# Kernel optimization log

Measured on AMD Instinct MI355X. Metric: run time of the kernel, lower is better.

## Reference

```python
import jax, jax.numpy as jnp
import numpy as np

L, B, D, H = 2048, 2, 1024, 16
DK = D // H
SCALE = DK ** -0.5


def setup_inputs() -> dict:
    key = jax.random.key(0)
    ks = jax.random.split(key, 11)
    w_std = D ** -0.5
    return {
        "query": jax.random.normal(ks[0], (L, B, D), dtype=jnp.float32),
        "key": jax.random.normal(ks[1], (L, B, D), dtype=jnp.float32),
        "value": jax.random.normal(ks[2], (L, B, D), dtype=jnp.float32),
        "WQ_w": jax.random.normal(ks[3], (D, D), dtype=jnp.float32) * w_std,
        "WQ_b": jnp.zeros((D,), dtype=jnp.float32),
        "WK_w": jax.random.normal(ks[4], (D, D), dtype=jnp.float32) * w_std,
        "WK_b": jnp.zeros((D,), dtype=jnp.float32),
        "WV_w": jax.random.normal(ks[5], (D, D), dtype=jnp.float32) * w_std,
        "WV_b": jnp.zeros((D,), dtype=jnp.float32),
        "WO_w": jax.random.normal(ks[6], (D, D), dtype=jnp.float32) * w_std,
        "WO_b": jnp.zeros((D,), dtype=jnp.float32),
    }


def reference(query, key, value, WQ_w, WQ_b, WK_w, WK_b, WV_w, WV_b, WO_w, WO_b):
    tgt_len, batch, _ = query.shape
    src_len = key.shape[0]
    # linear projections (torch Linear: x @ W^T + b)
    q = (query @ WQ_w.T + WQ_b) * SCALE            # [L, B, D]
    k = key @ WK_w.T + WK_b                        # [S, B, D]
    v = value @ WV_w.T + WV_b                      # [S, B, D]
    # split heads: [len, B, D] -> [B*H, len, DK]
    q = q.reshape(tgt_len, batch * H, DK).transpose(1, 0, 2)
    k = k.reshape(src_len, batch * H, DK).transpose(1, 0, 2)
    v = v.reshape(src_len, batch * H, DK).transpose(1, 0, 2)
    # attention scores and softmax (full [B*H, L, S] matrix, as in the original)
    scores = jnp.einsum('nld,nsd->nls', q, k)      # [B*H, L, S]
    probs = jax.nn.softmax(scores, axis=-1)
    out = jnp.einsum('nls,nsd->nld', probs, v)     # [B*H, L, DK]
    # merge heads: [B*H, L, DK] -> [L, B, D]
    out = out.transpose(1, 0, 2).reshape(tgt_len, batch, D)
    return out @ WO_w.T + WO_b
```

## Files before the change

kernel.cpp:

```cpp
#include <hip/hip_runtime.h>
#include <hip/hip_fp16.h>

#define LL 2048
#define BB 2
#define DD 1024
#define HH 16
#define DKK 64

typedef _Float16 h8 __attribute__((ext_vector_type(8)));
typedef _Float16 h4 __attribute__((ext_vector_type(4)));
typedef float f4 __attribute__((ext_vector_type(4)));
typedef float f16v __attribute__((ext_vector_type(16)));

#define BAR() do {                                              \
    asm volatile("s_waitcnt lgkmcnt(0)" ::: "memory");          \
    __builtin_amdgcn_s_barrier();                               \
    asm volatile("" ::: "memory");                              \
} while (0)

__device__ __forceinline__ void gload_lds16(const void* g, void* l) {
    __builtin_amdgcn_global_load_lds(
        (const __attribute__((address_space(1))) void*)g,
        (__attribute__((address_space(3))) void*)l, 16, 0, 0);
}

__device__ __forceinline__ unsigned pack2h(float a, float b) {
    union { _Float16 h[2]; unsigned u; } x;
    x.h[0] = (_Float16)a; x.h[1] = (_Float16)b;
    return x.u;
}

__global__ __launch_bounds__(256) void cvt_all(
    const float* __restrict__ x0, const float* __restrict__ x1,
    const float* __restrict__ x2, const float* __restrict__ w0,
    const float* __restrict__ w1, const float* __restrict__ w2,
    const float* __restrict__ w3,
    _Float16* __restrict__ y0, _Float16* __restrict__ y1,
    _Float16* __restrict__ y2, _Float16* __restrict__ z0,
    _Float16* __restrict__ z1, _Float16* __restrict__ z2,
    _Float16* __restrict__ z3)
{
    const int sel = blockIdx.y;
    if (sel >= 3 && blockIdx.x >= 512) return;
    const float* src = (sel == 0) ? x0 : (sel == 1) ? x1 : (sel == 2) ? x2
                     : (sel == 3) ? w0 : (sel == 4) ? w1 : (sel == 5) ? w2 : w3;
    _Float16* dst = (sel == 0) ? y0 : (sel == 1) ? y1 : (sel == 2) ? y2
                  : (sel == 3) ? z0 : (sel == 4) ? z1 : (sel == 5) ? z2 : z3;
    const int i = (blockIdx.x * 256 + threadIdx.x) * 8;
    f4 a = *(const f4*)(src + i);
    f4 b = *(const f4*)(src + i + 4);
    h8 o = {(_Float16)a.x, (_Float16)a.y, (_Float16)a.z, (_Float16)a.w,
            (_Float16)b.x, (_Float16)b.y, (_Float16)b.z, (_Float16)b.w};
    *(h8*)(dst + i) = o;
}

__global__ __launch_bounds__(256) void qkv_proj(
    const _Float16* __restrict__ xq, const _Float16* __restrict__ xk,
    const _Float16* __restrict__ xv,
    const _Float16* __restrict__ wq, const float* __restrict__ bq,
    const _Float16* __restrict__ wk, const float* __restrict__ bk,
    const _Float16* __restrict__ wv, const float* __restrict__ bv,
    _Float16* __restrict__ qh, _Float16* __restrict__ kh,
    _Float16* __restrict__ vth)
{
    const int mode = blockIdx.z;
    const _Float16* X    = (mode == 0) ? xq : (mode == 1) ? xk : xv;
    const _Float16* W    = (mode == 0) ? wq : (mode == 1) ? wk : wv;
    const float*    bias = (mode == 0) ? bq : (mode == 1) ? bk : bv;

    __shared__ alignas(16) _Float16 a_sm[128 * 32];
    __shared__ alignas(16) _Float16 b_sm[128 * 32];

    const int tid  = threadIdx.x;
    const int lane = tid & 63;
    const int wave = tid >> 6;
    const int wm = (wave & 1) * 64;
    const int wn = (wave >> 1) * 64;
    const int m0 = blockIdx.x * 128;
    const int n0 = blockIdx.y * 128;

    const int srow = tid >> 2;
    const int scol = (tid & 3) * 8;
    const int lds_base = wave * 512;

    f4 acc[4][4];
    #pragma unroll
    for (int i = 0; i < 4; i++)
        #pragma unroll
        for (int j = 0; j < 4; j++)
            #pragma unroll
            for (int r = 0; r < 4; r++) acc[i][j][r] = 0.f;

    const int fr = lane & 15;
    const int fk = (lane >> 4) * 8;

    for (int k0 = 0; k0 < DD; k0 += 32) {
        gload_lds16(X + (size_t)(m0 + srow) * DD + k0 + scol,       &a_sm[lds_base]);
        gload_lds16(X + (size_t)(m0 + 64 + srow) * DD + k0 + scol,  &a_sm[2048 + lds_base]);
        gload_lds16(W + (size_t)(n0 + srow) * DD + k0 + scol,       &b_sm[lds_base]);
        gload_lds16(W + (size_t)(n0 + 64 + srow) * DD + k0 + scol,  &b_sm[2048 + lds_base]);
        __syncthreads();
        h8 af[4], bfr[4];
        #pragma unroll
        for (int i = 0; i < 4; i++) af[i]  = *(const h8*)&a_sm[(wm + i * 16 + fr) * 32 + fk];
        #pragma unroll
        for (int j = 0; j < 4; j++) bfr[j] = *(const h8*)&b_sm[(wn + j * 16 + fr) * 32 + fk];
        #pragma unroll
        for (int i = 0; i < 4; i++)
            #pragma unroll
            for (int j = 0; j < 4; j++)
                acc[i][j] = __builtin_amdgcn_mfma_f32_16x16x32_f16(af[i], bfr[j], acc[i][j], 0, 0, 0);
        __syncthreads();
    }

    const int colc = lane & 15;
    const int rowb = (lane >> 4) * 4;
    #pragma unroll
    for (int i = 0; i < 4; i++) {
        #pragma unroll
        for (int j = 0; j < 4; j++) {
            const int nn = n0 + wn + j * 16 + colc;
            const float bval = bias[nn];
            #pragma unroll
            for (int reg = 0; reg < 4; reg++) {
                const int mm = m0 + wm + i * 16 + rowb + reg;
                float v = acc[i][j][reg] + bval;
                const int b = mm & 1, l = mm >> 1;
                const int h = nn >> 6, dk = nn & 63;
                const int head = b * HH + h;
                if (mode == 0) {
                    v *= 0.1803368801111243f;
                    qh[((size_t)head * LL + l) * DKK + dk] = (_Float16)v;
                } else if (mode == 1) {
                    kh[((size_t)head * LL + l) * DKK + dk] = (_Float16)v;
                } else {
                    vth[((size_t)head * DKK + dk) * LL + l] = (_Float16)v;
                }
            }
        }
    }
}

__global__ __launch_bounds__(256, 2) void attn(
    const _Float16* __restrict__ qh, const _Float16* __restrict__ kh,
    const _Float16* __restrict__ vth, _Float16* __restrict__ oh)
{
    const int head = blockIdx.y;
    const int q0   = blockIdx.x * 128;
    const int tid = threadIdx.x, lane = tid & 63, wave = tid >> 6;
    const int qw = q0 + wave * 32;

    __shared__ alignas(16) _Float16 k_sm[128][72];
    __shared__ alignas(16) _Float16 vt_sm[64][136];
    __shared__ float ls_sm[4][32];

    const int rq = lane & 31;
    const int hi = lane >> 5;
    const int kb = hi * 8;
    const int tid8 = tid * 8;

    const _Float16* khead  = kh  + (size_t)head * LL * DKK;
    const _Float16* vthead = vth + (size_t)head * DKK * LL;

    const _Float16* qbase = qh + ((size_t)head * LL + qw + rq) * DKK;
    h8 qa[4];
    #pragma unroll
    for (int kf = 0; kf < 4; kf++) qa[kf] = *(const h8*)(qbase + kf * 16 + kb);

    f16v o0, o1;
    #pragma unroll
    for (int r = 0; r < 16; r++) { o0[r] = 0.f; o1[r] = 0.f; }
    float lsum = 0.f;

    #pragma unroll
    for (int t = 0; t < 4; t++) {
        const int flat = t * 2048 + tid8;
        *(h8*)&k_sm[flat >> 6][flat & 63] = *(const h8*)(khead + flat);
        *(h8*)&vt_sm[flat >> 7][flat & 127] =
            *(const h8*)(vthead + (size_t)(flat >> 7) * LL + (flat & 127));
    }
    BAR();

    for (int it = 0; it < 16; ++it) {
        const int s1 = it * 128 + 128;
        const bool more = (s1 < LL);

        h8 kpre[4], vpre[4];
        if (more) {
            const _Float16* kg = khead + (size_t)s1 * DKK;
            #pragma unroll
            for (int t = 0; t < 4; t++) kpre[t] = *(const h8*)(kg + t * 2048 + tid8);
            #pragma unroll
            for (int t = 0; t < 4; t++) {
                const int flat = t * 2048 + tid8;
                vpre[t] = *(const h8*)(vthead + (size_t)(flat >> 7) * LL + s1 + (flat & 127));
            }
        }

        f16v sc[4];
        #pragma unroll
        for (int st = 0; st < 4; st++) {
            #pragma unroll
            for (int r = 0; r < 16; r++) sc[st][r] = 0.f;
            #pragma unroll
            for (int kf = 0; kf < 4; kf++) {
                h8 kf8 = *(const h8*)&k_sm[st * 32 + rq][kf * 16 + kb];
                sc[st] = __builtin_amdgcn_mfma_f32_32x32x16_f16(kf8, qa[kf], sc[st], 0, 0, 0);
            }
        }

        #pragma unroll
        for (int st = 0; st < 4; st++) {
            float p[16];
            #pragma unroll
            for (int r = 0; r < 16; r++) {
                p[r] = __builtin_amdgcn_exp2f(sc[st][r]);
                lsum += p[r];
            }
            unsigned own[4][2], part[4][2];
            #pragma unroll
            for (int g = 0; g < 4; g++) {
                own[g][0] = pack2h(p[4 * g],     p[4 * g + 1]);
                own[g][1] = pack2h(p[4 * g + 2], p[4 * g + 3]);
                part[g][0] = __shfl_xor(own[g][0], 32, 64);
                part[g][1] = __shfl_xor(own[g][1], 32, 64);
            }
            #pragma unroll
            for (int j = 0; j < 2; j++) {
                union { unsigned u[4]; h8 h; } pa;
                pa.u[0] = hi ? part[2 * j + 1][0] : own[2 * j][0];
                pa.u[1] = hi ? part[2 * j + 1][1] : own[2 * j][1];
                pa.u[2] = hi ? own[2 * j + 1][0]  : part[2 * j][0];
                pa.u[3] = hi ? own[2 * j + 1][1]  : part[2 * j][1];
                h8 b0 = *(const h8*)&vt_sm[rq][st * 32 + j * 16 + kb];
                h8 b1 = *(const h8*)&vt_sm[32 + rq][st * 32 + j * 16 + kb];
                o0 = __builtin_amdgcn_mfma_f32_32x32x16_f16(pa.h, b0, o0, 0, 0, 0);
                o1 = __builtin_amdgcn_mfma_f32_32x32x16_f16(pa.h, b1, o1, 0, 0, 0);
            }
        }

        BAR();
        if (more) {
            #pragma unroll
            for (int t = 0; t < 4; t++) {
                const int flat = t * 2048 + tid8;
                *(h8*)&k_sm[flat >> 6][flat & 63] = kpre[t];
            }
            #pragma unroll
            for (int t = 0; t < 4; t++) {
                const int flat = t * 2048 + tid8;
                *(h8*)&vt_sm[flat >> 7][flat & 127] = vpre[t];
            }
            BAR();
        }
    }

    lsum += __shfl_xor(lsum, 32, 64);
    ls_sm[wave][rq] = 1.0f / lsum;
    asm volatile("s_waitcnt lgkmcnt(0)" ::: "memory");

    const int b = head >> 4, h = head & 15;
    #pragma unroll
    for (int r = 0; r < 16; r++) {
        const int qrow = (r & 3) + 8 * (r >> 2) + 4 * hi;
        const float inv = ls_sm[wave][qrow];
        const int ql = qw + qrow;
        const size_t base = (size_t)(ql * BB + b) * DD + h * DKK;
        oh[base + rq]      = (_Float16)(o0[r] * inv);
        oh[base + 32 + rq] = (_Float16)(o1[r] * inv);
    }
}

__global__ __launch_bounds__(256) void out_proj(
    const _Float16* __restrict__ oh, const _Float16* __restrict__ wo,
    const float* __restrict__ bo, float* __restrict__ out)
{
    __shared__ alignas(16) _Float16 a_sm[64 * 32];
    __shared__ alignas(16) _Float16 b_sm[128 * 32];
    const int tid = threadIdx.x, lane = tid & 63, wave = tid >> 6;
    const int wm = (wave & 1) * 32, wn = (wave >> 1) * 64;
    const int m0 = blockIdx.x * 64, n0 = blockIdx.y * 128;

    const int srow = tid >> 2;
    const int scol = (tid & 3) * 8;
    const int lds_base = wave * 512;

    f4 acc[2][4];
    #pragma unroll
    for (int i = 0; i < 2; i++)
        #pragma unroll
        for (int j = 0; j < 4; j++)
            #pragma unroll
            for (int r = 0; r < 4; r++) acc[i][j][r] = 0.f;

    const int fr = lane & 15;
    const int fk = (lane >> 4) * 8;

    for (int k0 = 0; k0 < DD; k0 += 32) {
        gload_lds16(oh + (size_t)(m0 + srow) * DD + k0 + scol,      &a_sm[lds_base]);
        gload_lds16(wo + (size_t)(n0 + srow) * DD + k0 + scol,      &b_sm[lds_base]);
        gload_lds16(wo + (size_t)(n0 + 64 + srow) * DD + k0 + scol, &b_sm[2048 + lds_base]);
        __syncthreads();
        h8 af[2], bfr[4];
        #pragma unroll
        for (int i = 0; i < 2; i++) af[i]  = *(const h8*)&a_sm[(wm + i * 16 + fr) * 32 + fk];
        #pragma unroll
        for (int j = 0; j < 4; j++) bfr[j] = *(const h8*)&b_sm[(wn + j * 16 + fr) * 32 + fk];
        #pragma unroll
        for (int i = 0; i < 2; i++)
            #pragma unroll
            for (int j = 0; j < 4; j++)
                acc[i][j] = __builtin_amdgcn_mfma_f32_16x16x32_f16(af[i], bfr[j], acc[i][j], 0, 0, 0);
        __syncthreads();
    }

    const int colc = lane & 15;
    const int rowb = (lane >> 4) * 4;
    #pragma unroll
    for (int i = 0; i < 2; i++) {
        #pragma unroll
        for (int j = 0; j < 4; j++) {
            const int nn = n0 + wn + j * 16 + colc;
            const float bval = bo[nn];
            #pragma unroll
            for (int reg = 0; reg < 4; reg++) {
                const int mm = m0 + wm + i * 16 + rowb + reg;
                out[(size_t)mm * DD + nn] = acc[i][j][reg] + bval;
            }
        }
    }
}

extern "C" void kernel_launch(void* const* d_in, const int* in_sizes, int n_in,
                              void* d_out, int out_size, void* d_ws, size_t ws_size,
                              hipStream_t stream) {
    const float* qin = (const float*)d_in[0];
    const float* kin = (const float*)d_in[1];
    const float* vin = (const float*)d_in[2];
    const float* wq  = (const float*)d_in[3];
    const float* bq  = (const float*)d_in[4];
    const float* wk  = (const float*)d_in[5];
    const float* bk  = (const float*)d_in[6];
    const float* wv  = (const float*)d_in[7];
    const float* bv  = (const float*)d_in[8];
    const float* wo  = (const float*)d_in[9];
    const float* bo  = (const float*)d_in[10];

    const size_t seg = (size_t)32 * LL * DKK;
    _Float16* qh  = (_Float16*)d_ws;
    _Float16* kh  = qh + seg;
    _Float16* vth = kh + seg;
    _Float16* oh  = vth + seg;
    _Float16* wqh = oh + seg;
    _Float16* wkh = wqh + (size_t)DD * DD;
    _Float16* wvh = wkh + (size_t)DD * DD;
    _Float16* woh = wvh + (size_t)DD * DD;
    _Float16* xqh = woh + (size_t)DD * DD;
    _Float16* xkh = xqh + seg;
    _Float16* xvh = xkh + seg;

    hipLaunchKernelGGL(cvt_all, dim3(2048, 7), dim3(256), 0, stream,
                       qin, kin, vin, wq, wk, wv, wo,
                       xqh, xkh, xvh, wqh, wkh, wvh, woh);
    hipLaunchKernelGGL(qkv_proj, dim3(32, 8, 3), dim3(256), 0, stream,
                       xqh, xkh, xvh, wqh, bq, wkh, bk, wvh, bv, qh, kh, vth);
    hipLaunchKernelGGL(attn, dim3(16, 32), dim3(256), 0, stream, qh, kh, vth, oh);
    hipLaunchKernelGGL(out_proj, dim3(64, 8), dim3(256), 0, stream, oh, woh,
                       bo, (float*)d_out);
}
```

Baseline: 229.1 us.

## Split attention KV range across wave pairs and halve query tile per block

The attention kernel now gives each block 64 query rows instead of 128. The four waves form two pairs that each process half of every 128-key tile, doubling the grid to 1024 blocks and raising the launch-bounds occupancy target. Partial output accumulators and row sums from the second wave pair are combined through shared memory before normalisation and store. The fp16 packing of probabilities also switches to the packed round-toward-zero conversion intrinsic. The aim is higher occupancy and better latency hiding, at the cost of loading K/V twice as often per query and an extra LDS reduction step.

New measurement: 231.5 us. No clear change (+1.1%).

```diff
diff --git a/kernel.cpp b/kernel.cpp
--- a/kernel.cpp
+++ b/kernel.cpp
@@ -25,8 +25,8 @@
 }
 
 __device__ __forceinline__ unsigned pack2h(float a, float b) {
-    union { _Float16 h[2]; unsigned u; } x;
-    x.h[0] = (_Float16)a; x.h[1] = (_Float16)b;
+    union { __fp16 v __attribute__((ext_vector_type(2))); unsigned u; } x;
+    x.v = __builtin_amdgcn_cvt_pkrtz(a, b);
     return x.u;
 }
 
@@ -141,18 +141,20 @@
     }
 }
 
-__global__ __launch_bounds__(256, 2) void attn(
+__global__ __launch_bounds__(256, 4) void attn(
     const _Float16* __restrict__ qh, const _Float16* __restrict__ kh,
     const _Float16* __restrict__ vth, _Float16* __restrict__ oh)
 {
     const int head = blockIdx.y;
-    const int q0   = blockIdx.x * 128;
+    const int q0   = blockIdx.x * 64;
     const int tid = threadIdx.x, lane = tid & 63, wave = tid >> 6;
-    const int qw = q0 + wave * 32;
-
-    __shared__ alignas(16) _Float16 k_sm[128][72];
-    __shared__ alignas(16) _Float16 vt_sm[64][136];
-    __shared__ float ls_sm[4][32];
+    const int qs = wave & 1;
+    const int sw = wave >> 1;
+    const int qw = q0 + qs * 32;
+
+    __shared__ alignas(16) char smem[36864 + 512];
+    _Float16* ksm  = (_Float16*)smem;
+    _Float16* vtsm = (_Float16*)(smem + 18432);
 
     const int rq = lane & 31;
     const int hi = lane >> 5;
@@ -173,48 +175,54 @@
     float lsum = 0.f;
 
     #pragma unroll
-    for (int t = 0; t < 4; t++) {
-        const int flat = t * 2048 + tid8;
-        *(h8*)&k_sm[flat >> 6][flat & 63] = *(const h8*)(khead + flat);
-        *(h8*)&vt_sm[flat >> 7][flat & 127] =
-            *(const h8*)(vthead + (size_t)(flat >> 7) * LL + (flat & 127));
+    for (int b2 = 0; b2 < 2; b2++) {
+        #pragma unroll
+        for (int i = 0; i < 2; i++) {
+            const int flat = i * 2048 + tid8;
+            const int row = flat >> 6, col = flat & 63;
+            *(h8*)&ksm[b2 * 4608 + row * 72 + col] =
+                *(const h8*)(khead + (size_t)(b2 * 64 + row) * DKK + col);
+            *(h8*)&vtsm[b2 * 4608 + row * 72 + col] =
+                *(const h8*)(vthead + (size_t)row * LL + b2 * 64 + col);
+        }
     }
     BAR();
+
+    const int koff = sw * 4608;
 
     for (int it = 0; it < 16; ++it) {
         const int s1 = it * 128 + 128;
         const bool more = (s1 < LL);
 
-        h8 kpre[4], vpre[4];
+        h8 kpre[2][2], vpre[2][2];
         if (more) {
-            const _Float16* kg = khead + (size_t)s1 * DKK;
-            #pragma unroll
-            for (int t = 0; t < 4; t++) kpre[t] = *(const h8*)(kg + t * 2048 + tid8);
-            #pragma unroll
-            for (int t = 0; t < 4; t++) {
-                const int flat = t * 2048 + tid8;
-                vpre[t] = *(const h8*)(vthead + (size_t)(flat >> 7) * LL + s1 + (flat & 127));
-            }
-        }
-
-        f16v sc[4];
-        #pragma unroll
-        for (int st = 0; st < 4; st++) {
-            #pragma unroll
-            for (int r = 0; r < 16; r++) sc[st][r] = 0.f;
+            #pragma unroll
+            for (int b2 = 0; b2 < 2; b2++) {
+                #pragma unroll
+                for (int i = 0; i < 2; i++) {
+                    const int flat = i * 2048 + tid8;
+                    const int row = flat >> 6, col = flat & 63;
+                    kpre[b2][i] = *(const h8*)(khead + (size_t)(s1 + b2 * 64 + row) * DKK + col);
+                    vpre[b2][i] = *(const h8*)(vthead + (size_t)row * LL + s1 + b2 * 64 + col);
+                }
+            }
+        }
+
+        #pragma unroll
+        for (int st = 0; st < 2; st++) {
+            f16v sc;
+            #pragma unroll
+            for (int r = 0; r < 16; r++) sc[r] = 0.f;
             #pragma unroll
             for (int kf = 0; kf < 4; kf++) {
-                h8 kf8 = *(const h8*)&k_sm[st * 32 + rq][kf * 16 + kb];
-                sc[st] = __builtin_amdgcn_mfma_f32_32x32x16_f16(kf8, qa[kf], sc[st], 0, 0, 0);
-            }
-        }
-
-        #pragma unroll
-        for (int st = 0; st < 4; st++) {
+                h8 kf8 = *(const h8*)&ksm[koff + (st * 32 + rq) * 72 + kf * 16 + kb];
+                sc = __builtin_amdgcn_mfma_f32_32x32x16_f16(kf8, qa[kf], sc, 0, 0, 0);
+            }
+
             float p[16];
             #pragma unroll
             for (int r = 0; r < 16; r++) {
-                p[r] = __builtin_amdgcn_exp2f(sc[st][r]);
+                p[r] = __builtin_amdgcn_exp2f(sc[r]);
                 lsum += p[r];
             }
             unsigned own[4][2], part[4][2];
@@ -226,14 +234,15 @@
                 part[g][1] = __shfl_xor(own[g][1], 32, 64);
             }
             #pragma unroll
-            for (int j = 0; j < 2; j++) {
+            for (int f = 0; f < 2; f++) {
                 union { unsigned u[4]; h8 h; } pa;
-                pa.u[0] = hi ? part[2 * j + 1][0] : own[2 * j][0];
-                pa.u[1] = hi ? part[2 * j + 1][1] : own[2 * j][1];
-                pa.u[2] = hi ? own[2 * j + 1][0]  : part[2 * j][0];
-                pa.u[3] = hi ? own[2 * j + 1][1]  : part[2 * j][1];
-                h8 b0 = *(const h8*)&vt_sm[rq][st * 32 + j * 16 + kb];
-                h8 b1 = *(const h8*)&vt_sm[32 + rq][st * 32 + j * 16 + kb];
+                pa.u[0] = hi ? part[2 * f + 1][0] : own[2 * f][0];
+                pa.u[1] = hi ? part[2 * f + 1][1] : own[2 * f][1];
+                pa.u[2] = hi ? own[2 * f + 1][0]  : part[2 * f][0];
+                pa.u[3] = hi ? own[2 * f + 1][1]  : part[2 * f][1];
+                const int vcol = st * 32 + f * 16 + kb;
+                h8 b0 = *(const h8*)&vtsm[koff + rq * 72 + vcol];
+                h8 b1 = *(const h8*)&vtsm[koff + (32 + rq) * 72 + vcol];
                 o0 = __builtin_amdgcn_mfma_f32_32x32x16_f16(pa.h, b0, o0, 0, 0, 0);
                 o1 = __builtin_amdgcn_mfma_f32_32x32x16_f16(pa.h, b1, o1, 0, 0, 0);
             }
@@ -242,32 +251,51 @@
         BAR();
         if (more) {
             #pragma unroll
-            for (int t = 0; t < 4; t++) {
-                const int flat = t * 2048 + tid8;
-                *(h8*)&k_sm[flat >> 6][flat & 63] = kpre[t];
-            }
-            #pragma unroll
-            for (int t = 0; t < 4; t++) {
-                const int flat = t * 2048 + tid8;
-                *(h8*)&vt_sm[flat >> 7][flat & 127] = vpre[t];
+            for (int b2 = 0; b2 < 2; b2++) {
+                #pragma unroll
+                for (int i = 0; i < 2; i++) {
+                    const int flat = i * 2048 + tid8;
+                    const int row = flat >> 6, col = flat & 63;
+                    *(h8*)&ksm[b2 * 4608 + row * 72 + col]  = kpre[b2][i];
+                    *(h8*)&vtsm[b2 * 4608 + row * 72 + col] = vpre[b2][i];
+                }
             }
             BAR();
         }
     }
 
     lsum += __shfl_xor(lsum, 32, 64);
-    ls_sm[wave][rq] = 1.0f / lsum;
-    asm volatile("s_waitcnt lgkmcnt(0)" ::: "memory");
-
-    const int b = head >> 4, h = head & 15;
-    #pragma unroll
-    for (int r = 0; r < 16; r++) {
-        const int qrow = (r & 3) + 8 * (r >> 2) + 4 * hi;
-        const float inv = ls_sm[wave][qrow];
-        const int ql = qw + qrow;
-        const size_t base = (size_t)(ql * BB + b) * DD + h * DKK;
-        oh[base + rq]      = (_Float16)(o0[r] * inv);
-        oh[base + 32 + rq] = (_Float16)(o1[r] * inv);
+
+    float* comb = (float*)smem;
+    float* lsp  = (float*)(smem + 16384);
+    float* invp = (float*)(smem + 16640);
+
+    if (wave >= 2) {
+        float* c = comb + qs * 2048;
+        #pragma unroll
+        for (int r = 0; r < 16; r++) {
+            const int row = (r & 3) + 8 * (r >> 2) + 4 * hi;
+            c[row * 64 + rq]      = o0[r];
+            c[row * 64 + 32 + rq] = o1[r];
+        }
+        if (hi == 0) lsp[qs * 32 + rq] = lsum;
+    }
+    BAR();
+    if (wave < 2) {
+        lsum += lsp[qs * 32 + rq];
+        invp[qs * 32 + rq] = 1.0f / lsum;
+        asm volatile("s_waitcnt lgkmcnt(0)" ::: "memory");
+        const int b = head >> 4, h = head & 15;
+        const float* c = comb + qs * 2048;
+        #pragma unroll
+        for (int r = 0; r < 16; r++) {
+            const int row = (r & 3) + 8 * (r >> 2) + 4 * hi;
+            const float inv = invp[qs * 32 + row];
+            const int ql = qw + row;
+            const size_t base = (size_t)(ql * BB + b) * DD + h * DKK;
+            oh[base + rq]      = (_Float16)((o0[r] + c[row * 64 + rq]) * inv);
+            oh[base + 32 + rq] = (_Float16)((o1[r] + c[row * 64 + 32 + rq]) * inv);
+        }
     }
 }
 
@@ -364,7 +392,7 @@
                        xqh, xkh, xvh, wqh, wkh, wvh, woh);
     hipLaunchKernelGGL(qkv_proj, dim3(32, 8, 3), dim3(256), 0, stream,
                        xqh, xkh, xvh, wqh, bq, wkh, bk, wvh, bv, qh, kh, vth);
-    hipLaunchKernelGGL(attn, dim3(16, 32), dim3(256), 0, stream, qh, kh, vth, oh);
+    hipLaunchKernelGGL(attn, dim3(32, 32), dim3(256), 0, stream, qh, kh, vth, oh);
     hipLaunchKernelGGL(out_proj, dim3(64, 8), dim3(256), 0, stream, oh, woh,
                        bo, (float*)d_out);
 }
```
